# Optimization experiments

Measured on AMD Instinct MI355X. Metric: run time of the kernel, lower is better.

The kernel has to match this reference:

```python
import jax, jax.numpy as jnp
import numpy as np

# dims matching init_kwargs
E = 256        # obs dim
H = 128        # rnn_hidden_dim
NQ = 8         # n_quantiles (forward_type='policy')
QED = 64       # quantile_embed_dim
HEADS = 2      # hpn_head_num
HYP = 64       # hpn_hyper_dim
NA = 14        # n_actions
NAG = 8        # n_agents
B = 512        # episode batch


def setup_inputs() -> dict:
    key = jax.random.key(0)
    ks = jax.random.split(key, 16)
    def rn(k, shape, scale):
        return jax.random.normal(k, shape, dtype=jnp.float32) * scale
    inp = {
        "inputs": rn(ks[0], (B, NAG, E), 1.0),
        "hidden_state": rn(ks[1], (B * NAG, H), 1.0),
        "rnd_quantiles": jax.random.uniform(ks[2], (B, 1, NQ), dtype=jnp.float32),
        # fc1
        "fc1_w": rn(ks[3], (E, H), 1.0 / np.sqrt(E)),
        "fc1_b": jnp.zeros((H,), jnp.float32),
        # hypernet (2-layer MLP producing per-sample H x (H*HEADS) weights)
        "hyp_w1": rn(ks[4], (NQ, HYP), 1.0 / np.sqrt(NQ)),
        "hyp_b1": jnp.zeros((HYP,), jnp.float32),
        "hyp_w2": rn(ks[5], (HYP, H * H * HEADS), 1.0 / np.sqrt(HYP)),
        "hyp_b2": jnp.zeros((H * H * HEADS,), jnp.float32),
        # merger softmax weights [1, heads, H], init 1.0 as in module
        "merger_w": jnp.ones((1, HEADS, H), jnp.float32),
        # GRUCell params (PyTorch layout: [3H, in])
        "gru_wi": rn(ks[6], (3 * H, H), 1.0 / np.sqrt(H)),
        "gru_wh": rn(ks[7], (3 * H, H), 1.0 / np.sqrt(H)),
        "gru_bi": jnp.zeros((3 * H,), jnp.float32),
        "gru_bh": jnp.zeros((3 * H,), jnp.float32),
        # phi (quantile embedding linear)
        "phi_w": rn(ks[8], (QED, H), 1.0 / np.sqrt(QED)),
        "phi_b": jnp.zeros((H,), jnp.float32),
        # fc2
        "fc2_w": rn(ks[9], (H, NA), 1.0 / np.sqrt(H)),
        "fc2_b": jnp.zeros((NA,), jnp.float32),
    }
    return inp


def reference(inputs, hidden_state, rnd_quantiles, fc1_w, fc1_b,
              hyp_w1, hyp_b1, hyp_w2, hyp_b2, merger_w,
              gru_wi, gru_wh, gru_bi, gru_bh, phi_w, phi_b, fc2_w, fc2_b):
    b, a, e = inputs.shape
    bs = b * a
    # fc1 + relu
    x = jax.nn.relu(inputs.reshape(bs, e) @ fc1_w + fc1_b)          # [bs, H]
    # prev return distribution: first-call value = ones
    prev = jnp.ones((bs, NQ), dtype=inputs.dtype)
    # hypernet -> per-sample weights [bs, H, H*HEADS]
    hh = jax.nn.relu(prev @ hyp_w1 + hyp_b1)
    input_w = (hh @ hyp_w2 + hyp_b2).reshape(bs, H, H * HEADS)
    # batched matmul: [bs,1,H] @ [bs,H,H*HEADS] -> [bs, HEADS, H]
    emb = jnp.einsum('bi,bio->bo', x, input_w).reshape(bs, HEADS, H)
    # merger: softmax over head dim
    emb = jnp.sum(jax.nn.softmax(merger_w, axis=1) * emb, axis=1)   # [bs, H]
    x2 = jax.nn.relu(emb)
    # GRUCell (PyTorch semantics)
    hprev = hidden_state.reshape(-1, H)
    gi = x2 @ gru_wi.T + gru_bi
    gh = hprev @ gru_wh.T + gru_bh
    ir, iz, inn = jnp.split(gi, 3, axis=1)
    hr, hz, hn = jnp.split(gh, 3, axis=1)
    r = jax.nn.sigmoid(ir + hr)
    z = jax.nn.sigmoid(iz + hz)
    n = jnp.tanh(inn + r * hn)
    h = (1.0 - z) * n + z * hprev                                   # [bs, H]
    # IQN quantile embedding (forward_type='policy', grouped by agents)
    nq = NQ
    bsg = bs // NAG
    rq = rnd_quantiles.reshape(-1)                                  # [bsg*nq]
    h2 = jnp.broadcast_to(h[:, None, :], (bs, nq, H)).reshape(bs * nq, H)
    fid = jnp.arange(QED, dtype=inputs.dtype)                       # [QED]
    cos = jnp.cos(jnp.pi * fid[None, :] * rq[:, None])              # [bsg*nq, QED]
    q_phi = jax.nn.relu(cos @ phi_w + phi_b)                        # [bsg*nq, H]
    q_phi = jnp.broadcast_to(q_phi.reshape(bsg, 1, nq, H),
                             (bsg, NAG, nq, H)).reshape(bs * nq, H)
    q = (h2 * q_phi) @ fc2_w + fc2_b                                # [bs*nq, NA]
    q = q.reshape(bs, nq, NA).transpose(0, 2, 1)                    # [bs, NA, nq]
    sorted_q = jnp.sort(q, axis=2)
    return sorted_q, h, rq.reshape(bsg, nq)
```

## Files before the change

### kernel.cpp

```cpp
#include <hip/hip_runtime.h>
#include <math.h>

typedef __attribute__((ext_vector_type(8))) short short8;
typedef __attribute__((ext_vector_type(4))) float floatx4;

#define E_DIM 256
#define H_DIM 128
#define NQv 8
#define QEDv 64
#define HYPv 64
#define NAv 14
#define NAGv 8
#define W2COL 32768

#define OUT_H_OFF 458752
#define OUT_RQ_OFF 983040
#define WS_WEFF 0
#define WS_QPHI 16384
#define WS_PACK 540672
#define FB_W1  0
#define FB_WE  4096
#define FB_WI  6144
#define FB_WH  12288
#define FRAGS_TOTAL 18432

__device__ __forceinline__ unsigned short f2bf(float x) {
  unsigned u = __builtin_bit_cast(unsigned, x);
  u += 0x7FFFu + ((u >> 16) & 1u);
  return (unsigned short)(u >> 16);
}

__global__ __launch_bounds__(256) void k_weff(
    const float* __restrict__ hyp_w1, const float* __restrict__ hyp_b1,
    const float* __restrict__ hyp_w2, const float* __restrict__ hyp_b2,
    const float* __restrict__ merger_w, float* __restrict__ weff) {
  __shared__ float hh[HYPv];
  __shared__ float part[4][2][64];
  int t = threadIdx.x;
  if (t < HYPv) {
    float s = hyp_b1[t];
#pragma unroll
    for (int i = 0; i < NQv; ++i) s += hyp_w1[i * HYPv + t];
    hh[t] = fmaxf(s, 0.f);
  }
  __syncthreads();
  int w = t >> 6, lane = t & 63;
  int i = blockIdx.x >> 1;
  int cbase = (blockIdx.x & 1) * 64;
  int o0 = i * 256 + cbase + lane;
  float a0 = 0.f, a1 = 0.f;
#pragma unroll
  for (int jj = 0; jj < 16; ++jj) {
    int j = w * 16 + jj;
    float hj = hh[j];
    a0 = fmaf(hj, hyp_w2[j * W2COL + o0], a0);
    a1 = fmaf(hj, hyp_w2[j * W2COL + o0 + 128], a1);
  }
  part[w][0][lane] = a0;
  part[w][1][lane] = a1;
  __syncthreads();
  if (t < 64) {
    int c = cbase + t;
    float h0 = part[0][0][t] + part[1][0][t] + part[2][0][t] + part[3][0][t]
               + hyp_b2[i * 256 + c];
    float h1 = part[0][1][t] + part[1][1][t] + part[2][1][t] + part[3][1][t]
               + hyp_b2[i * 256 + c + 128];
    float m0 = merger_w[c], m1 = merger_w[128 + c];
    float mx = fmaxf(m0, m1);
    float e0 = expf(m0 - mx), e1 = expf(m1 - mx);
    weff[i * 128 + c] = (e0 * h0 + e1 * h1) / (e0 + e1);
  }
}

__global__ __launch_bounds__(256) void k_pack(
    const float* __restrict__ fc1_w, const float* __restrict__ weff,
    const float* __restrict__ gru_wi, const float* __restrict__ gru_wh,
    unsigned short* __restrict__ wp) {
  int f = blockIdx.x * 256 + threadIdx.x;
  if (f >= FRAGS_TOTAL) return;
  float v[8];
  if (f < FB_WE) {
    int g = f, kt = g >> 9, nt = (g >> 6) & 7, lane = g & 63;
    int k0 = kt * 32 + ((lane >> 4) << 3), n = nt * 16 + (lane & 15);
#pragma unroll
    for (int j = 0; j < 8; ++j) v[j] = fc1_w[(k0 + j) * H_DIM + n];
  } else if (f < FB_WI) {
    int g = f - FB_WE, kt = g >> 9, nt = (g >> 6) & 7, lane = g & 63;
    int k0 = kt * 32 + ((lane >> 4) << 3), n = nt * 16 + (lane & 15);
#pragma unroll
    for (int j = 0; j < 8; ++j) v[j] = weff[(k0 + j) * H_DIM + n];
  } else if (f < FB_WH) {
    int g = f - FB_WI, kt = g / 1536, rem = g % 1536, nt = rem >> 6, lane = rem & 63;
    int k0 = kt * 32 + ((lane >> 4) << 3), n = nt * 16 + (lane & 15);
#pragma unroll
    for (int j = 0; j < 8; ++j) v[j] = gru_wi[n * H_DIM + k0 + j];
  } else {
    int g = f - FB_WH, kt = g / 1536, rem = g % 1536, nt = rem >> 6, lane = rem & 63;
    int k0 = kt * 32 + ((lane >> 4) << 3), n = nt * 16 + (lane & 15);
#pragma unroll
    for (int j = 0; j < 8; ++j) v[j] = gru_wh[n * H_DIM + k0 + j];
  }
  short8 pk;
#pragma unroll
  for (int j = 0; j < 8; ++j) pk[j] = (short)f2bf(v[j]);
  *(short8*)(wp + (size_t)f * 8) = pk;
}

__global__ __launch_bounds__(256) void k_rnn(
    const float* __restrict__ inp, const float* __restrict__ hprev,
    const float* __restrict__ fc1_b, const unsigned short* __restrict__ wp,
    const float* __restrict__ gru_bi, const float* __restrict__ gru_bh,
    float* __restrict__ h_out) {
  __shared__ __align__(16) unsigned short lds_in[8][64][8];
  __shared__ __align__(16) unsigned short lds_x1[4][64][8];
  __shared__ __align__(16) unsigned short lds_x2[4][64][8];
  __shared__ __align__(16) unsigned short lds_h[4][64][8];
  int t = threadIdx.x;
  int b0 = blockIdx.x * 16;
  int lane = t & 63, w = t >> 6;

#pragma unroll
  for (int i = 0; i < 2; ++i) {
    int idx = i * 256 + t;
    int oct = idx & 31, m = idx >> 5;
    const float* p = inp + (size_t)(b0 + m) * E_DIM + oct * 8;
    floatx4 v0 = *(const floatx4*)p;
    floatx4 v1 = *(const floatx4*)(p + 4);
    short8 pk;
    pk[0] = (short)f2bf(v0.x); pk[1] = (short)f2bf(v0.y);
    pk[2] = (short)f2bf(v0.z); pk[3] = (short)f2bf(v0.w);
    pk[4] = (short)f2bf(v1.x); pk[5] = (short)f2bf(v1.y);
    pk[6] = (short)f2bf(v1.z); pk[7] = (short)f2bf(v1.w);
    *(short8*)&lds_in[oct >> 2][(oct & 3) * 16 + m][0] = pk;
  }
  {
    int oct = t & 15, m = t >> 4;
    const float* p = hprev + (size_t)(b0 + m) * H_DIM + oct * 8;
    floatx4 v0 = *(const floatx4*)p;
    floatx4 v1 = *(const floatx4*)(p + 4);
    short8 pk;
    pk[0] = (short)f2bf(v0.x); pk[1] = (short)f2bf(v0.y);
    pk[2] = (short)f2bf(v0.z); pk[3] = (short)f2bf(v0.w);
    pk[4] = (short)f2bf(v1.x); pk[5] = (short)f2bf(v1.y);
    pk[6] = (short)f2bf(v1.z); pk[7] = (short)f2bf(v1.w);
    *(short8*)&lds_h[oct >> 2][(oct & 3) * 16 + m][0] = pk;
  }
  __syncthreads();

  int nt0 = w * 2;
  {
    short8 aIn[8];
#pragma unroll
    for (int kt = 0; kt < 8; ++kt)
      aIn[kt] = *(const short8*)&lds_in[kt][lane][0];
    floatx4 c1[2] = {{0.f,0.f,0.f,0.f},{0.f,0.f,0.f,0.f}};
#pragma unroll
    for (int kt = 0; kt < 8; ++kt) {
#pragma unroll
      for (int n = 0; n < 2; ++n) {
        short8 b = *(const short8*)(wp +
            ((size_t)(FB_W1 + (kt * 8 + nt0 + n) * 64 + lane)) * 8);
        c1[n] = __builtin_amdgcn_mfma_f32_16x16x32_bf16(aIn[kt], b, c1[n], 0, 0, 0);
      }
    }
#pragma unroll
    for (int n = 0; n < 2; ++n) {
      int col = (nt0 + n) * 16 + (lane & 15);
      float bias = fc1_b[col];
#pragma unroll
      for (int reg = 0; reg < 4; ++reg) {
        float v = fmaxf(c1[n][reg] + bias, 0.f);
        int mm = (lane >> 4) * 4 + reg;
        lds_x1[col >> 5][((col >> 3) & 3) * 16 + mm][col & 7] = f2bf(v);
      }
    }
  }
  __syncthreads();

  {
    short8 a2[4];
#pragma unroll
    for (int kt = 0; kt < 4; ++kt)
      a2[kt] = *(const short8*)&lds_x1[kt][lane][0];
    floatx4 c2[2] = {{0.f,0.f,0.f,0.f},{0.f,0.f,0.f,0.f}};
#pragma unroll
    for (int kt = 0; kt < 4; ++kt) {
#pragma unroll
      for (int n = 0; n < 2; ++n) {
        short8 b = *(const short8*)(wp +
            ((size_t)(FB_WE + (kt * 8 + nt0 + n) * 64 + lane)) * 8);
        c2[n] = __builtin_amdgcn_mfma_f32_16x16x32_bf16(a2[kt], b, c2[n], 0, 0, 0);
      }
    }
#pragma unroll
    for (int n = 0; n < 2; ++n) {
      int col = (nt0 + n) * 16 + (lane & 15);
#pragma unroll
      for (int reg = 0; reg < 4; ++reg) {
        float v = fmaxf(c2[n][reg], 0.f);
        int mm = (lane >> 4) * 4 + reg;
        lds_x2[col >> 5][((col >> 3) & 3) * 16 + mm][col & 7] = f2bf(v);
      }
    }
  }
  __syncthreads();

  {
    short8 ax[4], ah[4];
#pragma unroll
    for (int kt = 0; kt < 4; ++kt) {
      ax[kt] = *(const short8*)&lds_x2[kt][lane][0];
      ah[kt] = *(const short8*)&lds_h[kt][lane][0];
    }
#pragma unroll
    for (int cti = 0; cti < 2; ++cti) {
      int ct = w + cti * 4;
      floatx4 giR = {0.f,0.f,0.f,0.f}, giZ = {0.f,0.f,0.f,0.f}, giN = {0.f,0.f,0.f,0.f};
      floatx4 ghR = {0.f,0.f,0.f,0.f}, ghZ = {0.f,0.f,0.f,0.f}, ghN = {0.f,0.f,0.f,0.f};
#pragma unroll
      for (int kt = 0; kt < 4; ++kt) {
        short8 bR = *(const short8*)(wp + ((size_t)(FB_WI + (kt * 24 + ct) * 64 + lane)) * 8);
        short8 bZ = *(const short8*)(wp + ((size_t)(FB_WI + (kt * 24 + ct + 8) * 64 + lane)) * 8);
        short8 bN = *(const short8*)(wp + ((size_t)(FB_WI + (kt * 24 + ct + 16) * 64 + lane)) * 8);
        short8 cR = *(const short8*)(wp + ((size_t)(FB_WH + (kt * 24 + ct) * 64 + lane)) * 8);
        short8 cZ = *(const short8*)(wp + ((size_t)(FB_WH + (kt * 24 + ct + 8) * 64 + lane)) * 8);
        short8 cN = *(const short8*)(wp + ((size_t)(FB_WH + (kt * 24 + ct + 16) * 64 + lane)) * 8);
        giR = __builtin_amdgcn_mfma_f32_16x16x32_bf16(ax[kt], bR, giR, 0, 0, 0);
        giZ = __builtin_amdgcn_mfma_f32_16x16x32_bf16(ax[kt], bZ, giZ, 0, 0, 0);
        giN = __builtin_amdgcn_mfma_f32_16x16x32_bf16(ax[kt], bN, giN, 0, 0, 0);
        ghR = __builtin_amdgcn_mfma_f32_16x16x32_bf16(ah[kt], cR, ghR, 0, 0, 0);
        ghZ = __builtin_amdgcn_mfma_f32_16x16x32_bf16(ah[kt], cZ, ghZ, 0, 0, 0);
        ghN = __builtin_amdgcn_mfma_f32_16x16x32_bf16(ah[kt], cN, ghN, 0, 0, 0);
      }
      int c = ct * 16 + (lane & 15);
      float bir = gru_bi[c], biz = gru_bi[128 + c], bin = gru_bi[256 + c];
      float bhr = gru_bh[c], bhz = gru_bh[128 + c], bhn = gru_bh[256 + c];
#pragma unroll
      for (int reg = 0; reg < 4; ++reg) {
        int row = b0 + (lane >> 4) * 4 + reg;
        float r = 1.f / (1.f + expf(-(giR[reg] + bir + ghR[reg] + bhr)));
        float z = 1.f / (1.f + expf(-(giZ[reg] + biz + ghZ[reg] + bhz)));
        float n = tanhf(giN[reg] + bin + r * (ghN[reg] + bhn));
        float hp = hprev[(size_t)row * H_DIM + c];
        h_out[(size_t)row * H_DIM + c] = (1.f - z) * n + z * hp;
      }
    }
  }
}

__global__ __launch_bounds__(128) void k_qphi(
    const float* __restrict__ rnd, const float* __restrict__ phi_w,
    const float* __restrict__ phi_b, float* __restrict__ qphi,
    float* __restrict__ rq_out) {
  const int R = 8;
  __shared__ float cos_s[R][QEDv];
  int t = threadIdx.x;
  int r0 = blockIdx.x * R;
#pragma unroll
  for (int ii = 0; ii < R * QEDv / 128; ++ii) {
    int idx = t + ii * 128;
    int r = idx >> 6, f = idx & 63;
    cos_s[r][f] = cosf(3.14159265358979323846f * (float)f * rnd[r0 + r]);
  }
  if (t < R) rq_out[r0 + t] = rnd[r0 + t];
  __syncthreads();
  float acc[R];
  float bv = phi_b[t];
#pragma unroll
  for (int r = 0; r < R; ++r) acc[r] = bv;
#pragma unroll 4
  for (int f = 0; f < QEDv; ++f) {
    float wv = phi_w[f * H_DIM + t];
#pragma unroll
    for (int r = 0; r < R; ++r) acc[r] = fmaf(cos_s[r][f], wv, acc[r]);
  }
#pragma unroll
  for (int r = 0; r < R; ++r)
    qphi[(size_t)(r0 + r) * H_DIM + t] = fmaxf(acc[r], 0.f);
}

__global__ __launch_bounds__(256) void k_qsort(
    const float* __restrict__ h_in, const float* __restrict__ qphi,
    const float* __restrict__ fc2_w, const float* __restrict__ fc2_b,
    float* __restrict__ q_out) {
  const int BB = 16;
  __shared__ float h_s[BB][H_DIM + 4];
  __shared__ float qp_s[BB][H_DIM + 4];
  __shared__ float w_s[NAv][H_DIM + 1];
  __shared__ float b_s[NAv];
  int t = threadIdx.x;
  int b0 = blockIdx.x * BB;
  {
    const float4* hs = (const float4*)(h_in + (size_t)b0 * H_DIM);
    for (int idx = t; idx < BB * H_DIM / 4; idx += 256) {
      int row = idx >> 5, col = idx & 31;
      ((float4*)&h_s[row][0])[col] = hs[idx];
    }
    const float4* qs = (const float4*)(qphi + (size_t)(b0 / NAGv) * NQv * H_DIM);
    for (int idx = t; idx < BB * H_DIM / 4; idx += 256) {
      int row = idx >> 5, col = idx & 31;
      ((float4*)&qp_s[row][0])[col] = qs[idx];
    }
    for (int idx = t; idx < H_DIM * NAv; idx += 256) {
      int cc = idx / NAv, aa = idx - cc * NAv;
      w_s[aa][cc] = fc2_w[idx];
    }
    if (t < NAv) b_s[t] = fc2_b[t];
  }
  __syncthreads();
  if (t >= BB * NAv) return;
  int bl = t / NAv, a = t - bl * NAv;
  int glb = (bl >> 3) << 3;
  float qv[NQv];
  float bias = b_s[a];
#pragma unroll
  for (int k = 0; k < NQv; ++k) qv[k] = bias;
  for (int cc = 0; cc < H_DIM; ++cc) {
    float hw = h_s[bl][cc] * w_s[a][cc];
#pragma unroll
    for (int k = 0; k < NQv; ++k)
      qv[k] = fmaf(hw, qp_s[glb + k][cc], qv[k]);
  }
#define CE(i, j) { float lo_ = fminf(qv[i], qv[j]); float hi_ = fmaxf(qv[i], qv[j]); qv[i] = lo_; qv[j] = hi_; }
  CE(0,1) CE(2,3) CE(4,5) CE(6,7)
  CE(0,2) CE(1,3) CE(4,6) CE(5,7)
  CE(1,2) CE(5,6)
  CE(0,4) CE(1,5) CE(2,6) CE(3,7)
  CE(2,4) CE(3,5)
  CE(1,2) CE(3,4) CE(5,6)
#undef CE
  float4* o4 = (float4*)(q_out + (size_t)((b0 + bl) * NAv + a) * NQv);
  o4[0] = make_float4(qv[0], qv[1], qv[2], qv[3]);
  o4[1] = make_float4(qv[4], qv[5], qv[6], qv[7]);
}

extern "C" void kernel_launch(void* const* d_in, const int* in_sizes, int n_in,
                              void* d_out, int out_size, void* d_ws, size_t ws_size,
                              hipStream_t stream) {
  (void)in_sizes; (void)n_in; (void)out_size; (void)ws_size;
  const float* inp      = (const float*)d_in[0];
  const float* hidden   = (const float*)d_in[1];
  const float* rnd      = (const float*)d_in[2];
  const float* fc1_w    = (const float*)d_in[3];
  const float* fc1_b    = (const float*)d_in[4];
  const float* hyp_w1   = (const float*)d_in[5];
  const float* hyp_b1   = (const float*)d_in[6];
  const float* hyp_w2   = (const float*)d_in[7];
  const float* hyp_b2   = (const float*)d_in[8];
  const float* merger_w = (const float*)d_in[9];
  const float* gru_wi   = (const float*)d_in[10];
  const float* gru_wh   = (const float*)d_in[11];
  const float* gru_bi   = (const float*)d_in[12];
  const float* gru_bh   = (const float*)d_in[13];
  const float* phi_w    = (const float*)d_in[14];
  const float* phi_b    = (const float*)d_in[15];
  const float* fc2_w    = (const float*)d_in[16];
  const float* fc2_b    = (const float*)d_in[17];
  float* out  = (float*)d_out;
  float* ws   = (float*)d_ws;
  float* weff = ws + WS_WEFF;
  float* qphi = ws + WS_QPHI;
  unsigned short* wp = (unsigned short*)(ws + WS_PACK);
  float* h_out = out + OUT_H_OFF;

  k_weff<<<dim3(256), dim3(256), 0, stream>>>(hyp_w1, hyp_b1, hyp_w2, hyp_b2,
                                              merger_w, weff);
  k_pack<<<dim3(72), dim3(256), 0, stream>>>(fc1_w, weff, gru_wi, gru_wh, wp);
  k_qphi<<<dim3(512), dim3(128), 0, stream>>>(rnd, phi_w, phi_b, qphi,
                                              out + OUT_RQ_OFF);
  k_rnn<<<dim3(256), dim3(256), 0, stream>>>(inp, hidden, fc1_b, wp,
                                             gru_bi, gru_bh, h_out);
  k_qsort<<<dim3(256), dim3(256), 0, stream>>>(h_out, qphi, fc2_w, fc2_b, out);
}
```

Baseline: 126.2 us.

## Fuse quantile embedding and fc2/sort into RNN kernel with MFMA

Merges the qphi and qsort kernels into the main RNN kernel. Each block now computes its own cosine embedding and phi projection with bf16 MFMA, and the fc2 quantile product and sort use MFMA over LDS-resident h and q_phi. The hypernet kernel writes the packed bf16 weight fragments directly, which removes the weff round trip through k_pack, and launches drop from five to three. In exchange, q_phi is recomputed per block, the elementwise product and the fc2 weights drop to bf16 precision, and __cosf is used in place of the accurate cosf.

```diff
diff --git a/kernel.cpp b/kernel.cpp
--- a/kernel.cpp
+++ b/kernel.cpp
@@ -15,25 +15,37 @@
 
 #define OUT_H_OFF 458752
 #define OUT_RQ_OFF 983040
-#define WS_WEFF 0
-#define WS_QPHI 16384
-#define WS_PACK 540672
+
 #define FB_W1  0
 #define FB_WE  4096
 #define FB_WI  6144
 #define FB_WH  12288
-#define FRAGS_TOTAL 18432
+#define FB_PHI 18432
+#define FB_FC2 19456
+#define PACK_UNITS 17664
+
+#define SM_IN   0
+#define SM_X1   8192
+#define SM_X2   12288
+#define SM_H    16384
+#define SM_PART 0
+#define SM_HF   32768
+#define SM_QP   41216
+#define SM_TOTAL 45568
 
 __device__ __forceinline__ unsigned short f2bf(float x) {
   unsigned u = __builtin_bit_cast(unsigned, x);
   u += 0x7FFFu + ((u >> 16) & 1u);
   return (unsigned short)(u >> 16);
 }
+__device__ __forceinline__ float bf2f(unsigned short s) {
+  return __builtin_bit_cast(float, ((unsigned)s) << 16);
+}
 
 __global__ __launch_bounds__(256) void k_weff(
     const float* __restrict__ hyp_w1, const float* __restrict__ hyp_b1,
     const float* __restrict__ hyp_w2, const float* __restrict__ hyp_b2,
-    const float* __restrict__ merger_w, float* __restrict__ weff) {
+    const float* __restrict__ merger_w, unsigned short* __restrict__ wp) {
   __shared__ float hh[HYPv];
   __shared__ float part[4][2][64];
   int t = threadIdx.x;
@@ -68,37 +80,50 @@
     float m0 = merger_w[c], m1 = merger_w[128 + c];
     float mx = fmaxf(m0, m1);
     float e0 = expf(m0 - mx), e1 = expf(m1 - mx);
-    weff[i * 128 + c] = (e0 * h0 + e1 * h1) / (e0 + e1);
+    float val = (e0 * h0 + e1 * h1) / (e0 + e1);
+    int unit = FB_WE + ((i >> 5) * 8 + (c >> 4)) * 64 + ((i >> 3) & 3) * 16 + (c & 15);
+    wp[(size_t)unit * 8 + (i & 7)] = f2bf(val);
   }
 }
 
 __global__ __launch_bounds__(256) void k_pack(
-    const float* __restrict__ fc1_w, const float* __restrict__ weff,
-    const float* __restrict__ gru_wi, const float* __restrict__ gru_wh,
-    unsigned short* __restrict__ wp) {
-  int f = blockIdx.x * 256 + threadIdx.x;
-  if (f >= FRAGS_TOTAL) return;
+    const float* __restrict__ fc1_w, const float* __restrict__ gru_wi,
+    const float* __restrict__ gru_wh, const float* __restrict__ phi_w,
+    const float* __restrict__ fc2_w, unsigned short* __restrict__ wp) {
+  int u = blockIdx.x * 256 + threadIdx.x;
+  if (u >= PACK_UNITS) return;
   float v[8];
-  if (f < FB_WE) {
-    int g = f, kt = g >> 9, nt = (g >> 6) & 7, lane = g & 63;
+  int f;
+  if (u < 4096) {
+    int g = u, nt = (g >> 6) & 7, lane = g & 63;
+    int k0 = (g >> 9) * 32 + ((lane >> 4) << 3), n = nt * 16 + (lane & 15);
+    f = FB_W1 + g;
+#pragma unroll
+    for (int j = 0; j < 8; ++j) v[j] = fc1_w[(k0 + j) * H_DIM + n];
+  } else if (u < 10240) {
+    int g = u - 4096, kt = g / 1536, rem = g % 1536, nt = rem >> 6, lane = rem & 63;
     int k0 = kt * 32 + ((lane >> 4) << 3), n = nt * 16 + (lane & 15);
-#pragma unroll
-    for (int j = 0; j < 8; ++j) v[j] = fc1_w[(k0 + j) * H_DIM + n];
-  } else if (f < FB_WI) {
-    int g = f - FB_WE, kt = g >> 9, nt = (g >> 6) & 7, lane = g & 63;
+    f = FB_WI + g;
+#pragma unroll
+    for (int j = 0; j < 8; ++j) v[j] = gru_wi[n * H_DIM + k0 + j];
+  } else if (u < 16384) {
+    int g = u - 10240, kt = g / 1536, rem = g % 1536, nt = rem >> 6, lane = rem & 63;
     int k0 = kt * 32 + ((lane >> 4) << 3), n = nt * 16 + (lane & 15);
-#pragma unroll
-    for (int j = 0; j < 8; ++j) v[j] = weff[(k0 + j) * H_DIM + n];
-  } else if (f < FB_WH) {
-    int g = f - FB_WI, kt = g / 1536, rem = g % 1536, nt = rem >> 6, lane = rem & 63;
+    f = FB_WH + g;
+#pragma unroll
+    for (int j = 0; j < 8; ++j) v[j] = gru_wh[n * H_DIM + k0 + j];
+  } else if (u < 17408) {
+    int g = u - 16384, kt = g >> 9, nt = (g >> 6) & 7, lane = g & 63;
     int k0 = kt * 32 + ((lane >> 4) << 3), n = nt * 16 + (lane & 15);
-#pragma unroll
-    for (int j = 0; j < 8; ++j) v[j] = gru_wi[n * H_DIM + k0 + j];
+    f = FB_PHI + g;
+#pragma unroll
+    for (int j = 0; j < 8; ++j) v[j] = phi_w[(k0 + j) * H_DIM + n];
   } else {
-    int g = f - FB_WH, kt = g / 1536, rem = g % 1536, nt = rem >> 6, lane = rem & 63;
-    int k0 = kt * 32 + ((lane >> 4) << 3), n = nt * 16 + (lane & 15);
-#pragma unroll
-    for (int j = 0; j < 8; ++j) v[j] = gru_wh[n * H_DIM + k0 + j];
+    int g = u - 17408, kt = g >> 6, lane = g & 63;
+    int k0 = kt * 32 + ((lane >> 4) << 3), n = lane & 15;
+    f = FB_FC2 + g;
+#pragma unroll
+    for (int j = 0; j < 8; ++j) v[j] = (n < NAv) ? fc2_w[(k0 + j) * NAv + n] : 0.f;
   }
   short8 pk;
 #pragma unroll
@@ -106,18 +131,29 @@
   *(short8*)(wp + (size_t)f * 8) = pk;
 }
 
-__global__ __launch_bounds__(256) void k_rnn(
+__global__ __launch_bounds__(256) void k_main(
     const float* __restrict__ inp, const float* __restrict__ hprev,
-    const float* __restrict__ fc1_b, const unsigned short* __restrict__ wp,
+    const float* __restrict__ rnd, const float* __restrict__ fc1_b,
+    const unsigned short* __restrict__ wp,
     const float* __restrict__ gru_bi, const float* __restrict__ gru_bh,
-    float* __restrict__ h_out) {
-  __shared__ __align__(16) unsigned short lds_in[8][64][8];
-  __shared__ __align__(16) unsigned short lds_x1[4][64][8];
-  __shared__ __align__(16) unsigned short lds_x2[4][64][8];
-  __shared__ __align__(16) unsigned short lds_h[4][64][8];
+    const float* __restrict__ phi_b, const float* __restrict__ fc2_b,
+    float* __restrict__ h_out, float* __restrict__ q_out,
+    float* __restrict__ rq_out) {
+  __shared__ __align__(16) char smem[SM_TOTAL];
+  unsigned short (*lds_in)[64][8] = (unsigned short(*)[64][8])(smem + SM_IN);
+  unsigned short (*lds_x1)[64][8] = (unsigned short(*)[64][8])(smem + SM_X1);
+  unsigned short (*lds_x2)[64][8] = (unsigned short(*)[64][8])(smem + SM_X2);
+  unsigned short (*lds_h)[64][8]  = (unsigned short(*)[64][8])(smem + SM_H);
+  float (*lds_hf)[132]            = (float(*)[132])(smem + SM_HF);
+  unsigned short (*lds_qp)[136]   = (unsigned short(*)[136])(smem + SM_QP);
+  float* lds_part                 = (float*)(smem + SM_PART);
+
   int t = threadIdx.x;
   int b0 = blockIdx.x * 16;
   int lane = t & 63, w = t >> 6;
+  int quad = lane >> 4, l16 = lane & 15;
+
+  if (t < 16) rq_out[b0 + t] = rnd[b0 + t];
 
 #pragma unroll
   for (int i = 0; i < 2; ++i) {
@@ -145,6 +181,39 @@
     pk[6] = (short)f2bf(v1.z); pk[7] = (short)f2bf(v1.w);
     *(short8*)&lds_h[oct >> 2][(oct & 3) * 16 + m][0] = pk;
   }
+
+  {
+    float rqv = rnd[b0 + l16];
+    short8 aC[2];
+#pragma unroll
+    for (int kt = 0; kt < 2; ++kt) {
+#pragma unroll
+      for (int j = 0; j < 8; ++j) {
+        float f = (float)(kt * 32 + quad * 8 + j);
+        aC[kt][j] = (short)f2bf(__cosf(3.14159265358979f * f * rqv));
+      }
+    }
+    floatx4 cP[2] = {{0.f,0.f,0.f,0.f},{0.f,0.f,0.f,0.f}};
+#pragma unroll
+    for (int kt = 0; kt < 2; ++kt) {
+#pragma unroll
+      for (int ni = 0; ni < 2; ++ni) {
+        int nt = w * 2 + ni;
+        short8 b = *(const short8*)(wp + ((size_t)(FB_PHI + (kt * 8 + nt) * 64 + lane)) * 8);
+        cP[ni] = __builtin_amdgcn_mfma_f32_16x16x32_bf16(aC[kt], b, cP[ni], 0, 0, 0);
+      }
+    }
+#pragma unroll
+    for (int ni = 0; ni < 2; ++ni) {
+      int col = (w * 2 + ni) * 16 + l16;
+      float bias = phi_b[col];
+#pragma unroll
+      for (int reg = 0; reg < 4; ++reg) {
+        int m_qp = quad * 4 + reg;
+        lds_qp[m_qp][col] = f2bf(fmaxf(cP[ni][reg] + bias, 0.f));
+      }
+    }
+  }
   __syncthreads();
 
   int nt0 = w * 2;
@@ -158,20 +227,18 @@
     for (int kt = 0; kt < 8; ++kt) {
 #pragma unroll
       for (int n = 0; n < 2; ++n) {
-        short8 b = *(const short8*)(wp +
-            ((size_t)(FB_W1 + (kt * 8 + nt0 + n) * 64 + lane)) * 8);
+        short8 b = *(const short8*)(wp + ((size_t)(FB_W1 + (kt * 8 + nt0 + n) * 64 + lane)) * 8);
         c1[n] = __builtin_amdgcn_mfma_f32_16x16x32_bf16(aIn[kt], b, c1[n], 0, 0, 0);
       }
     }
 #pragma unroll
     for (int n = 0; n < 2; ++n) {
-      int col = (nt0 + n) * 16 + (lane & 15);
+      int col = (nt0 + n) * 16 + l16;
       float bias = fc1_b[col];
 #pragma unroll
       for (int reg = 0; reg < 4; ++reg) {
         float v = fmaxf(c1[n][reg] + bias, 0.f);
-        int mm = (lane >> 4) * 4 + reg;
-        lds_x1[col >> 5][((col >> 3) & 3) * 16 + mm][col & 7] = f2bf(v);
+        lds_x1[col >> 5][((col >> 3) & 3) * 16 + quad * 4 + reg][col & 7] = f2bf(v);
       }
     }
   }
@@ -187,19 +254,17 @@
     for (int kt = 0; kt < 4; ++kt) {
 #pragma unroll
       for (int n = 0; n < 2; ++n) {
-        short8 b = *(const short8*)(wp +
-            ((size_t)(FB_WE + (kt * 8 + nt0 + n) * 64 + lane)) * 8);
+        short8 b = *(const short8*)(wp + ((size_t)(FB_WE + (kt * 8 + nt0 + n) * 64 + lane)) * 8);
         c2[n] = __builtin_amdgcn_mfma_f32_16x16x32_bf16(a2[kt], b, c2[n], 0, 0, 0);
       }
     }
 #pragma unroll
     for (int n = 0; n < 2; ++n) {
-      int col = (nt0 + n) * 16 + (lane & 15);
+      int col = (nt0 + n) * 16 + l16;
 #pragma unroll
       for (int reg = 0; reg < 4; ++reg) {
         float v = fmaxf(c2[n][reg], 0.f);
-        int mm = (lane >> 4) * 4 + reg;
-        lds_x2[col >> 5][((col >> 3) & 3) * 16 + mm][col & 7] = f2bf(v);
+        lds_x2[col >> 5][((col >> 3) & 3) * 16 + quad * 4 + reg][col & 7] = f2bf(v);
       }
     }
   }
@@ -232,106 +297,80 @@
         ghZ = __builtin_amdgcn_mfma_f32_16x16x32_bf16(ah[kt], cZ, ghZ, 0, 0, 0);
         ghN = __builtin_amdgcn_mfma_f32_16x16x32_bf16(ah[kt], cN, ghN, 0, 0, 0);
       }
-      int c = ct * 16 + (lane & 15);
+      int c = ct * 16 + l16;
       float bir = gru_bi[c], biz = gru_bi[128 + c], bin = gru_bi[256 + c];
       float bhr = gru_bh[c], bhz = gru_bh[128 + c], bhn = gru_bh[256 + c];
 #pragma unroll
       for (int reg = 0; reg < 4; ++reg) {
-        int row = b0 + (lane >> 4) * 4 + reg;
+        int rl = quad * 4 + reg;
+        int row = b0 + rl;
         float r = 1.f / (1.f + expf(-(giR[reg] + bir + ghR[reg] + bhr)));
         float z = 1.f / (1.f + expf(-(giZ[reg] + biz + ghZ[reg] + bhz)));
         float n = tanhf(giN[reg] + bin + r * (ghN[reg] + bhn));
         float hp = hprev[(size_t)row * H_DIM + c];
-        h_out[(size_t)row * H_DIM + c] = (1.f - z) * n + z * hp;
-      }
-    }
-  }
-}
-
-__global__ __launch_bounds__(128) void k_qphi(
-    const float* __restrict__ rnd, const float* __restrict__ phi_w,
-    const float* __restrict__ phi_b, float* __restrict__ qphi,
-    float* __restrict__ rq_out) {
-  const int R = 8;
-  __shared__ float cos_s[R][QEDv];
-  int t = threadIdx.x;
-  int r0 = blockIdx.x * R;
-#pragma unroll
-  for (int ii = 0; ii < R * QEDv / 128; ++ii) {
-    int idx = t + ii * 128;
-    int r = idx >> 6, f = idx & 63;
-    cos_s[r][f] = cosf(3.14159265358979323846f * (float)f * rnd[r0 + r]);
-  }
-  if (t < R) rq_out[r0 + t] = rnd[r0 + t];
-  __syncthreads();
-  float acc[R];
-  float bv = phi_b[t];
-#pragma unroll
-  for (int r = 0; r < R; ++r) acc[r] = bv;
-#pragma unroll 4
-  for (int f = 0; f < QEDv; ++f) {
-    float wv = phi_w[f * H_DIM + t];
-#pragma unroll
-    for (int r = 0; r < R; ++r) acc[r] = fmaf(cos_s[r][f], wv, acc[r]);
-  }
-#pragma unroll
-  for (int r = 0; r < R; ++r)
-    qphi[(size_t)(r0 + r) * H_DIM + t] = fmaxf(acc[r], 0.f);
-}
-
-__global__ __launch_bounds__(256) void k_qsort(
-    const float* __restrict__ h_in, const float* __restrict__ qphi,
-    const float* __restrict__ fc2_w, const float* __restrict__ fc2_b,
-    float* __restrict__ q_out) {
-  const int BB = 16;
-  __shared__ float h_s[BB][H_DIM + 4];
-  __shared__ float qp_s[BB][H_DIM + 4];
-  __shared__ float w_s[NAv][H_DIM + 1];
-  __shared__ float b_s[NAv];
-  int t = threadIdx.x;
-  int b0 = blockIdx.x * BB;
-  {
-    const float4* hs = (const float4*)(h_in + (size_t)b0 * H_DIM);
-    for (int idx = t; idx < BB * H_DIM / 4; idx += 256) {
-      int row = idx >> 5, col = idx & 31;
-      ((float4*)&h_s[row][0])[col] = hs[idx];
-    }
-    const float4* qs = (const float4*)(qphi + (size_t)(b0 / NAGv) * NQv * H_DIM);
-    for (int idx = t; idx < BB * H_DIM / 4; idx += 256) {
-      int row = idx >> 5, col = idx & 31;
-      ((float4*)&qp_s[row][0])[col] = qs[idx];
-    }
-    for (int idx = t; idx < H_DIM * NAv; idx += 256) {
-      int cc = idx / NAv, aa = idx - cc * NAv;
-      w_s[aa][cc] = fc2_w[idx];
-    }
-    if (t < NAv) b_s[t] = fc2_b[t];
-  }
-  __syncthreads();
-  if (t >= BB * NAv) return;
-  int bl = t / NAv, a = t - bl * NAv;
-  int glb = (bl >> 3) << 3;
-  float qv[NQv];
-  float bias = b_s[a];
-#pragma unroll
-  for (int k = 0; k < NQv; ++k) qv[k] = bias;
-  for (int cc = 0; cc < H_DIM; ++cc) {
-    float hw = h_s[bl][cc] * w_s[a][cc];
-#pragma unroll
-    for (int k = 0; k < NQv; ++k)
-      qv[k] = fmaf(hw, qp_s[glb + k][cc], qv[k]);
-  }
+        float hv = (1.f - z) * n + z * hp;
+        h_out[(size_t)row * H_DIM + c] = hv;
+        lds_hf[rl][c] = hv;
+      }
+    }
+  }
+  __syncthreads();
+
+  {
+    int m = l16;
+    int k0 = w * 32 + quad * 8;
+    const float* hptr = &lds_hf[m][k0];
+    floatx4 h0 = *(const floatx4*)hptr;
+    floatx4 h1 = *(const floatx4*)(hptr + 4);
+    float hf[8] = {h0.x, h0.y, h0.z, h0.w, h1.x, h1.y, h1.z, h1.w};
+    short8 bF = *(const short8*)(wp + ((size_t)(FB_FC2 + w * 64 + lane)) * 8);
+    int qbase = (m >> 3) * 8;
+    floatx4 cQ[8];
+#pragma unroll
+    for (int q = 0; q < NQv; ++q) cQ[q] = (floatx4){0.f,0.f,0.f,0.f};
+#pragma unroll
+    for (int q = 0; q < NQv; ++q) {
+      short8 qpv = *(const short8*)&lds_qp[qbase + q][k0];
+      short8 au;
+#pragma unroll
+      for (int j = 0; j < 8; ++j)
+        au[j] = (short)f2bf(hf[j] * bf2f((unsigned short)qpv[j]));
+      cQ[q] = __builtin_amdgcn_mfma_f32_16x16x32_bf16(au, bF, cQ[q], 0, 0, 0);
+    }
+#pragma unroll
+    for (int q = 0; q < NQv; ++q)
+      *(floatx4*)&lds_part[((w * 8 + q) * 64 + lane) * 4] = cQ[q];
+  }
+  __syncthreads();
+
+  {
+    int s = t >> 4, a = t & 15;
+    int pl = (s >> 2) * 16 + a;
+    int pr = s & 3;
+    float bias = (a < NAv) ? fc2_b[a] : 0.f;
+    float qv[NQv];
+#pragma unroll
+    for (int q = 0; q < NQv; ++q) {
+      float acc = bias;
+#pragma unroll
+      for (int ww = 0; ww < 4; ++ww)
+        acc += lds_part[((ww * 8 + q) * 64 + pl) * 4 + pr];
+      qv[q] = acc;
+    }
 #define CE(i, j) { float lo_ = fminf(qv[i], qv[j]); float hi_ = fmaxf(qv[i], qv[j]); qv[i] = lo_; qv[j] = hi_; }
-  CE(0,1) CE(2,3) CE(4,5) CE(6,7)
-  CE(0,2) CE(1,3) CE(4,6) CE(5,7)
-  CE(1,2) CE(5,6)
-  CE(0,4) CE(1,5) CE(2,6) CE(3,7)
-  CE(2,4) CE(3,5)
-  CE(1,2) CE(3,4) CE(5,6)
+    CE(0,1) CE(2,3) CE(4,5) CE(6,7)
+    CE(0,2) CE(1,3) CE(4,6) CE(5,7)
+    CE(1,2) CE(5,6)
+    CE(0,4) CE(1,5) CE(2,6) CE(3,7)
+    CE(2,4) CE(3,5)
+    CE(1,2) CE(3,4) CE(5,6)
 #undef CE
-  float4* o4 = (float4*)(q_out + (size_t)((b0 + bl) * NAv + a) * NQv);
-  o4[0] = make_float4(qv[0], qv[1], qv[2], qv[3]);
-  o4[1] = make_float4(qv[4], qv[5], qv[6], qv[7]);
+    if (a < NAv) {
+      float4* o4 = (float4*)(q_out + (size_t)((b0 + s) * NAv + a) * NQv);
+      o4[0] = make_float4(qv[0], qv[1], qv[2], qv[3]);
+      o4[1] = make_float4(qv[4], qv[5], qv[6], qv[7]);
+    }
+  }
 }
 
 extern "C" void kernel_launch(void* const* d_in, const int* in_sizes, int n_in,
@@ -357,18 +396,14 @@
   const float* fc2_w    = (const float*)d_in[16];
   const float* fc2_b    = (const float*)d_in[17];
   float* out  = (float*)d_out;
-  float* ws   = (float*)d_ws;
-  float* weff = ws + WS_WEFF;
-  float* qphi = ws + WS_QPHI;
-  unsigned short* wp = (unsigned short*)(ws + WS_PACK);
+  unsigned short* wp = (unsigned short*)d_ws;
   float* h_out = out + OUT_H_OFF;
 
+  k_pack<<<dim3(69), dim3(256), 0, stream>>>(fc1_w, gru_wi, gru_wh, phi_w,
+                                             fc2_w, wp);
   k_weff<<<dim3(256), dim3(256), 0, stream>>>(hyp_w1, hyp_b1, hyp_w2, hyp_b2,
-                                              merger_w, weff);
-  k_pack<<<dim3(72), dim3(256), 0, stream>>>(fc1_w, weff, gru_wi, gru_wh, wp);
-  k_qphi<<<dim3(512), dim3(128), 0, stream>>>(rnd, phi_w, phi_b, qphi,
-                                              out + OUT_RQ_OFF);
-  k_rnn<<<dim3(256), dim3(256), 0, stream>>>(inp, hidden, fc1_b, wp,
-                                             gru_bi, gru_bh, h_out);
-  k_qsort<<<dim3(256), dim3(256), 0, stream>>>(h_out, qphi, fc2_w, fc2_b, out);
-}
+                                              merger_w, wp);
+  k_main<<<dim3(256), dim3(256), 0, stream>>>(inp, hidden, rnd, fc1_b, wp,
+                                              gru_bi, gru_bh, phi_b, fc2_b,
+                                              h_out, out, out + OUT_RQ_OFF);
+}
```

Result: faster. 109.4 us (-13.3%).
